# Performance work log

Hardware: AMD Instinct MI355X
Metric: run time of the kernel (lower is better)

## Reference

```python
import jax, jax.numpy as jnp
import numpy as np


def setup_inputs() -> dict:
    key = jax.random.key(0)
    k1, k2 = jax.random.split(key, 2)
    B, N, D = 8, 2048, 1024
    x = jax.random.normal(k1, (B, N, D), dtype=jnp.float32)
    # Linear(D, 3D): weight stored as [in, out] for x @ W
    W_qkv = jax.random.normal(k2, (D, 3 * D), dtype=jnp.float32) * (D ** -0.5)
    b_qkv = jnp.zeros((3 * D,), dtype=jnp.float32)
    return {"x": x, "W_qkv": W_qkv, "b_qkv": b_qkv}


def reference(x, W_qkv, b_qkv):
    D = x.shape[-1]
    scale = D ** -0.5
    qkv = x @ W_qkv + b_qkv                      # [B, N, 3D]
    q, k, v = jnp.split(qkv, 3, axis=-1)         # each [B, N, D]
    # attention scores: note original scales AFTER matmul (same math)
    atten = jnp.einsum('bnd,bmd->bnm', q, k) * scale  # [B, N, N]
    atten = jax.nn.softmax(atten, axis=-1)
    out = jnp.einsum('bnm,bmd->bnd', atten, v)   # [B, N, D]
    return out
```

## Files before the change

kernel.cpp:

```cpp
#include <hip/hip_runtime.h>
#include <hip/hip_bf16.h>


typedef __attribute__((ext_vector_type(8))) short bf16x8;
typedef __attribute__((ext_vector_type(4))) float f32x4;
typedef __attribute__((ext_vector_type(8))) unsigned short u16x8;
typedef __attribute__((address_space(1))) const unsigned int gu32;
typedef __attribute__((address_space(3))) unsigned int lu32;

__device__ __forceinline__ unsigned short f2bf(float f) {
  union { float f; unsigned int u; } v; v.f = f;
  unsigned int r = v.u + 0x7fffu + ((v.u >> 16) & 1u);
  return (unsigned short)(r >> 16);
}
__device__ __forceinline__ void cp16(const unsigned short* g, unsigned short* l) {
  __builtin_amdgcn_global_load_lds((gu32*)g, (lu32*)l, 16, 0, 0);
}

__global__ __launch_bounds__(256) void prep(const float* __restrict__ x,
                                            unsigned short* __restrict__ xb,
                                            const float* __restrict__ W,
                                            unsigned short* __restrict__ Wt,
                                            float* __restrict__ rowsum) {
  __shared__ unsigned short tile[64][72];
  int bid = blockIdx.x, t = threadIdx.x;
  if (bid < 8192) {
    long i = ((long)bid * 256 + t) * 8;
    float4 a = *(const float4*)(x + i);
    float4 b = *(const float4*)(x + i + 4);
    u16x8 o;
    o[0] = f2bf(a.x); o[1] = f2bf(a.y); o[2] = f2bf(a.z); o[3] = f2bf(a.w);
    o[4] = f2bf(b.x); o[5] = f2bf(b.y); o[6] = f2bf(b.z); o[7] = f2bf(b.w);
    *(u16x8*)(xb + i) = o;
  } else if (bid < 8960) {
    int wb = bid - 8192;
    int fb = wb % 48, db = wb / 48;
#pragma unroll
    for (int it = 0; it < 4; it++) {
      int c = t + it * 256;
      int r = c >> 4, c4 = (c & 15) * 4;
      float4 v = *(const float4*)(W + (long)(db * 64 + r) * 3072 + fb * 64 + c4);
      tile[r][c4 + 0] = f2bf(v.x); tile[r][c4 + 1] = f2bf(v.y);
      tile[r][c4 + 2] = f2bf(v.z); tile[r][c4 + 3] = f2bf(v.w);
    }
    __syncthreads();
#pragma unroll
    for (int it = 0; it < 2; it++) {
      int c = t + it * 256;
      int r2 = c >> 3, k8 = (c & 7) * 8;
      u16x8 o;
#pragma unroll
      for (int j = 0; j < 8; j++) o[j] = tile[k8 + j][r2];
      *(u16x8*)(Wt + (long)(fb * 64 + r2) * 1024 + db * 64 + k8) = o;
    }
  } else {
    rowsum[(bid - 8960) * 256 + t] = 0.f;
  }
}

template <int MODE, int SWZ>
__global__ __launch_bounds__(256) void gemm_nt(
    const unsigned short* __restrict__ A, const unsigned short* __restrict__ B,
    float* __restrict__ C, const float* __restrict__ bias, int Ncols, int K, float scale,
    unsigned short* __restrict__ qp, unsigned short* __restrict__ kp,
    unsigned short* __restrict__ vp, float* __restrict__ rsum,
    long strA, long strB, long strC) {
  __shared__ __align__(16) unsigned short As[128 * 64];
  __shared__ __align__(16) unsigned short Bs[128 * 64];
  const int tid = threadIdx.x;
  const int lane = tid & 63, wave = tid >> 6;
  const int quad = lane >> 4, l16 = lane & 15;
  const int bz = blockIdx.z;
  int mt, nt;
  if (SWZ == 0) {
    mt = blockIdx.y; nt = blockIdx.x;
  } else {
    int bid = blockIdx.x;
    int w = bid & 15, st = bid >> 4;
    constexpr int NSUP = SWZ / 4;
    mt = (st / NSUP) * 4 + (w >> 2);
    nt = (st % NSUP) * 4 + (w & 3);
  }
  const long m0 = (long)mt * 128;
  const int n0 = nt * 128;
  const int wm = (wave >> 1) * 64, wn = (wave & 1) * 64;
  const int w8 = wave * 8;
  const int lr = lane >> 3;
  const int swz = (lane & 7) ^ lr;

  f32x4 zero = {0.f, 0.f, 0.f, 0.f};
  f32x4 acc[4][4];
#pragma unroll
  for (int i = 0; i < 4; i++)
#pragma unroll
    for (int j = 0; j < 4; j++) acc[i][j] = zero;

  const unsigned short* aSt = A + (long)bz * strA + (m0 + w8 + lr) * (long)K + swz * 8;
  const unsigned short* bSt = B + (long)bz * strB + ((long)(n0 + w8 + lr)) * K + swz * 8;
  unsigned short* lA = As + (w8 * 64) + lane * 8;
  unsigned short* lB = Bs + (w8 * 64) + lane * 8;

  for (int k0 = 0; k0 < K; k0 += 64) {
    __syncthreads();
#pragma unroll
    for (int j = 0; j < 4; j++) {
      cp16(aSt + (long)j * 32 * K + k0, lA + j * 32 * 64);
      cp16(bSt + (long)j * 32 * K + k0, lB + j * 32 * 64);
    }
    __syncthreads();
#pragma unroll
    for (int h = 0; h < 2; h++) {
      bf16x8 af[4], bfr[4];
#pragma unroll
      for (int i = 0; i < 4; i++) {
        int row = wm + i * 16 + l16;
        af[i] = *(const bf16x8*)(As + row * 64 + (((h << 2) | quad) ^ (row & 7)) * 8);
      }
#pragma unroll
      for (int j = 0; j < 4; j++) {
        int row = wn + j * 16 + l16;
        bfr[j] = *(const bf16x8*)(Bs + row * 64 + (((h << 2) | quad) ^ (row & 7)) * 8);
      }
#pragma unroll
      for (int i = 0; i < 4; i++)
#pragma unroll
        for (int j = 0; j < 4; j++)
          acc[i][j] = __builtin_amdgcn_mfma_f32_16x16x32_bf16(af[i], bfr[j], acc[i][j], 0, 0, 0);
    }
  }

  if (MODE == 1) {
#pragma unroll
    for (int j = 0; j < 4; j++) {
      int fg = n0 + wn + j * 16 + l16;
      float bv = bias[fg];
      if (fg < 2048) {
        unsigned short* outp = (fg < 1024) ? qp : kp;
        int fo = fg & 1023;
#pragma unroll
        for (int i = 0; i < 4; i++)
#pragma unroll
          for (int r = 0; r < 4; r++) {
            long t = m0 + wm + i * 16 + quad * 4 + r;
            outp[t * 1024 + fo] = f2bf(acc[i][j][r] + bv);
          }
      } else {
        int d = fg - 2048;
#pragma unroll
        for (int i = 0; i < 4; i++)
#pragma unroll
          for (int r = 0; r < 4; r++) {
            long t = m0 + wm + i * 16 + quad * 4 + r;
            vp[((long)(t >> 11) * 1024 + d) * 2048 + (t & 2047)] = f2bf(acc[i][j][r] + bv);
          }
      }
    }
  } else if (MODE == 3) {
    unsigned short* Co = qp + (long)bz * strC;
    float* rs = rsum + bz * 2048;
#pragma unroll
    for (int i = 0; i < 4; i++)
#pragma unroll
      for (int r = 0; r < 4; r++) {
        long gm = m0 + wm + i * 16 + quad * 4 + r;
        float psum = 0.f;
#pragma unroll
        for (int j = 0; j < 4; j++) {
          float e = __expf(acc[i][j][r] * scale);
          psum += e;
          Co[gm * Ncols + n0 + wn + j * 16 + l16] = f2bf(e);
        }
        psum += __shfl_xor(psum, 1);
        psum += __shfl_xor(psum, 2);
        psum += __shfl_xor(psum, 4);
        psum += __shfl_xor(psum, 8);
        if (l16 == 0) atomicAdd(rs + gm, psum);
      }
  } else {
    float* Co = C + (long)bz * strC;
    const float* rs = rsum + bz * 2048;
#pragma unroll
    for (int i = 0; i < 4; i++)
#pragma unroll
      for (int r = 0; r < 4; r++) {
        long gm = m0 + wm + i * 16 + quad * 4 + r;
        float inv = 1.0f / rs[gm];
#pragma unroll
        for (int j = 0; j < 4; j++)
          Co[gm * Ncols + n0 + wn + j * 16 + l16] = acc[i][j][r] * inv;
      }
  }
}

extern "C" void kernel_launch(void* const* d_in, const int* in_sizes, int n_in,
                              void* d_out, int out_size, void* d_ws, size_t ws_size,
                              hipStream_t stream) {
  const float* x = (const float*)d_in[0];
  const float* W = (const float*)d_in[1];
  const float* bq = (const float*)d_in[2];
  float* out = (float*)d_out;
  char* ws = (char*)d_ws;
  const long MB = 1L << 20;
  unsigned short* Q  = (unsigned short*)(ws);
  unsigned short* Kb = (unsigned short*)(ws + 32 * MB);
  unsigned short* Vt = (unsigned short*)(ws + 64 * MB);
  unsigned short* xb = (unsigned short*)(ws + 96 * MB);
  unsigned short* Wt = (unsigned short*)(ws + 128 * MB);
  unsigned short* E  = (unsigned short*)(ws + 96 * MB);
  float* rowsum      = (float*)(ws + 160 * MB);

  prep<<<9024, 256, 0, stream>>>(x, xb, W, Wt, rowsum);
  gemm_nt<1, 0><<<dim3(24, 128, 1), 256, 0, stream>>>(xb, Wt, nullptr, bq, 3072, 1024, 1.0f,
                                                      Q, Kb, Vt, nullptr, 0, 0, 0);
  gemm_nt<3, 16><<<dim3(256, 1, 8), 256, 0, stream>>>(Q, Kb, nullptr, nullptr, 2048, 1024,
                                                      0.03125f, E, nullptr, nullptr, rowsum,
                                                      2048L * 1024, 2048L * 1024, 2048L * 2048);
  gemm_nt<4, 8><<<dim3(128, 1, 8), 256, 0, stream>>>(E, Vt, out, nullptr, 1024, 2048, 1.0f,
                                                     nullptr, nullptr, nullptr, rowsum,
                                                     2048L * 2048, 1024L * 2048, 2048L * 1024);
}
```

Measured before the change: 402.6 us.

## Use 256x256 double-buffered GEMM tiles with interleaved async LDS prefetch

Replaces the 128x128 single-buffered GEMM with a 512-thread kernel that computes 256x256 output tiles per block. It keeps two LDS buffers and issues global-to-LDS copies for the next K-tiles between MFMA phases, using explicit waitcnt, barriers and s_setprio. The launch grids and tile swizzles for all three GEMMs are adjusted to match. The goal is more data reuse per LDS load and latency hiding for the global loads. In exchange the kernel uses much more LDS and registers, which lowers occupancy, and the attention GEMMs now launch fewer blocks.

```diff
diff --git a/kernel.cpp b/kernel.cpp
--- a/kernel.cpp
+++ b/kernel.cpp
@@ -59,17 +59,18 @@
 }
 
 template <int MODE, int SWZ>
-__global__ __launch_bounds__(256) void gemm_nt(
+__global__ __launch_bounds__(512, 2) void gemm256(
     const unsigned short* __restrict__ A, const unsigned short* __restrict__ B,
     float* __restrict__ C, const float* __restrict__ bias, int Ncols, int K, float scale,
     unsigned short* __restrict__ qp, unsigned short* __restrict__ kp,
     unsigned short* __restrict__ vp, float* __restrict__ rsum,
     long strA, long strB, long strC) {
-  __shared__ __align__(16) unsigned short As[128 * 64];
-  __shared__ __align__(16) unsigned short Bs[128 * 64];
+  __shared__ __align__(16) unsigned short As[2][256 * 64];
+  __shared__ __align__(16) unsigned short Bs[2][256 * 64];
   const int tid = threadIdx.x;
   const int lane = tid & 63, wave = tid >> 6;
   const int quad = lane >> 4, l16 = lane & 15;
+  const int lr = lane >> 3, lc = lane & 7;
   const int bz = blockIdx.z;
   int mt, nt;
   if (SWZ == 0) {
@@ -77,81 +78,130 @@
   } else {
     int bid = blockIdx.x;
     int w = bid & 15, st = bid >> 4;
-    constexpr int NSUP = SWZ / 4;
+    constexpr int NSUP = (SWZ >= 4) ? (SWZ / 4) : 1;
     mt = (st / NSUP) * 4 + (w >> 2);
     nt = (st % NSUP) * 4 + (w & 3);
   }
-  const long m0 = (long)mt * 128;
-  const int n0 = nt * 128;
-  const int wm = (wave >> 1) * 64, wn = (wave & 1) * 64;
-  const int w8 = wave * 8;
-  const int lr = lane >> 3;
-  const int swz = (lane & 7) ^ lr;
-
+  const long m0 = (long)mt * 256;
+  const int n0 = nt * 256;
+  const int wm128 = (wave >> 2) * 128;
+  const int wn64 = (wave & 3) * 64;
+  const int NT = K >> 6, mask = NT - 1;
+
+  const unsigned short* __restrict__ Ab = A + (long)bz * strA;
+  const unsigned short* __restrict__ Bb = B + (long)bz * strB;
+
+  unsigned int aSrc[4], bSrc[4];
+  int aOff[4], bOff[4];
+  {
+    const int auL[4] = {0, 128, 64, 192}, auH[4] = {32, 160, 96, 224};
+    const int buL[4] = {0, 128, 32, 160}, buH[4] = {64, 192, 96, 224};
+    const bool wlo = wave < 4;
+    const int w8 = (wave & 3) * 8;
+    const int sc = (lc ^ lr) * 8;
+#pragma unroll
+    for (int u = 0; u < 4; u++) {
+      int ra = (wlo ? auL[u] : auH[u]) + w8 + lr;
+      int rb = (wlo ? buL[u] : buH[u]) + w8 + lr;
+      aSrc[u] = (unsigned int)(((int)m0 + ra) * K + sc);
+      bSrc[u] = (unsigned int)((n0 + rb) * K + sc);
+      aOff[u] = ra * 64 + lc * 8;
+      bOff[u] = rb * 64 + lc * 8;
+    }
+  }
+
+#define SA(u, bb, tt) cp16(Ab + aSrc[u] + (tt) * 64, &As[bb][aOff[u]])
+#define SB(u, bb, tt) cp16(Bb + bSrc[u] + (tt) * 64, &Bs[bb][bOff[u]])
+
+  f32x4 acc[8][4];
   f32x4 zero = {0.f, 0.f, 0.f, 0.f};
-  f32x4 acc[4][4];
-#pragma unroll
-  for (int i = 0; i < 4; i++)
+#pragma unroll
+  for (int i = 0; i < 8; i++)
 #pragma unroll
     for (int j = 0; j < 4; j++) acc[i][j] = zero;
-
-  const unsigned short* aSt = A + (long)bz * strA + (m0 + w8 + lr) * (long)K + swz * 8;
-  const unsigned short* bSt = B + (long)bz * strB + ((long)(n0 + w8 + lr)) * K + swz * 8;
-  unsigned short* lA = As + (w8 * 64) + lane * 8;
-  unsigned short* lB = Bs + (w8 * 64) + lane * 8;
-
-  for (int k0 = 0; k0 < K; k0 += 64) {
-    __syncthreads();
+  bf16x8 am[4][2], bn[4][2];
+
+  SA(0, 0, 0); SA(1, 0, 0); SB(0, 0, 0); SB(1, 0, 0);
+  SA(2, 0, 0); SA(3, 0, 0); SB(2, 0, 0); SB(3, 0, 0);
+  SA(0, 1, 1); SA(1, 1, 1); SB(0, 1, 1); SB(1, 1, 1);
+  SA(2, 1, 1); SA(3, 1, 1);
+  asm volatile("s_waitcnt vmcnt(6)" ::: "memory");
+  __builtin_amdgcn_s_barrier();
+
+#define RD_A(bb, mg)                                                                        \
+  _Pragma("unroll") for (int ii = 0; ii < 4; ii++) {                                        \
+    int row = wm128 + ((mg) * 4 + ii) * 16 + l16;                                           \
+    _Pragma("unroll") for (int h = 0; h < 2; h++)                                           \
+      am[ii][h] = *(const bf16x8*)(&As[bb][row * 64 + ((((h << 2) | quad)) ^ (row & 7)) * 8]); \
+  }
+#define RD_B(bb, ng)                                                                        \
+  _Pragma("unroll") for (int jj = 0; jj < 2; jj++) {                                        \
+    int row = wn64 + ((ng) * 2 + jj) * 16 + l16;                                            \
+    _Pragma("unroll") for (int h = 0; h < 2; h++)                                           \
+      bn[(ng) * 2 + jj][h] = *(const bf16x8*)(&Bs[bb][row * 64 + ((((h << 2) | quad)) ^ (row & 7)) * 8]); \
+  }
+#define MM(mg, ng)                                                                          \
+  _Pragma("unroll") for (int ii = 0; ii < 4; ii++)                                          \
+    _Pragma("unroll") for (int jj = 0; jj < 2; jj++)                                        \
+      _Pragma("unroll") for (int h = 0; h < 2; h++)                                         \
+        acc[(mg) * 4 + ii][(ng) * 2 + jj] = __builtin_amdgcn_mfma_f32_16x16x32_bf16(        \
+            am[ii][h], bn[(ng) * 2 + jj][h], acc[(mg) * 4 + ii][(ng) * 2 + jj], 0, 0, 0);
+#define BARRIER __builtin_amdgcn_s_barrier()
+#define LGKM0 asm volatile("s_waitcnt lgkmcnt(0)" ::: "memory")
+#define PRIO1 __builtin_amdgcn_s_setprio(1)
+#define PRIO0 __builtin_amdgcn_s_setprio(0)
+
+#define TILE(bb, tt)                                                                        \
+  {                                                                                         \
+    const int t1_ = ((tt) + 1) & mask, t2_ = ((tt) + 2) & mask;                             \
+                                          \
+    RD_A(bb, 0); RD_B(bb, 0);                                                               \
+    SB(2, (bb) ^ 1, t1_); SB(3, (bb) ^ 1, t1_);                                             \
+    BARRIER; LGKM0; PRIO1; MM(0, 0); PRIO0; BARRIER;                                        \
+                     \
+    RD_B(bb, 1);                                                                            \
+    SA(0, bb, t2_); SA(1, bb, t2_);                                                         \
+    BARRIER; LGKM0; PRIO1; MM(0, 1); PRIO0; BARRIER;                                        \
+                                     \
+    RD_A(bb, 1);                                                                            \
+    SB(0, bb, t2_); SB(1, bb, t2_);                                                         \
+    BARRIER; LGKM0; PRIO1; MM(1, 0); PRIO0; BARRIER;                                        \
+           \
+    SA(2, bb, t2_); SA(3, bb, t2_);                                                         \
+    BARRIER; PRIO1; MM(1, 1); PRIO0;                                                        \
+    asm volatile("s_waitcnt vmcnt(6)" ::: "memory");                                        \
+    BARRIER;                                                                                \
+  }
+
+#pragma unroll 1
+  for (int t = 0; t < NT; t += 2) {
+    TILE(0, t);
+    TILE(1, t + 1);
+  }
+
+  if (MODE == 1) {
 #pragma unroll
     for (int j = 0; j < 4; j++) {
-      cp16(aSt + (long)j * 32 * K + k0, lA + j * 32 * 64);
-      cp16(bSt + (long)j * 32 * K + k0, lB + j * 32 * 64);
-    }
-    __syncthreads();
-#pragma unroll
-    for (int h = 0; h < 2; h++) {
-      bf16x8 af[4], bfr[4];
-#pragma unroll
-      for (int i = 0; i < 4; i++) {
-        int row = wm + i * 16 + l16;
-        af[i] = *(const bf16x8*)(As + row * 64 + (((h << 2) | quad) ^ (row & 7)) * 8);
-      }
-#pragma unroll
-      for (int j = 0; j < 4; j++) {
-        int row = wn + j * 16 + l16;
-        bfr[j] = *(const bf16x8*)(Bs + row * 64 + (((h << 2) | quad) ^ (row & 7)) * 8);
-      }
-#pragma unroll
-      for (int i = 0; i < 4; i++)
-#pragma unroll
-        for (int j = 0; j < 4; j++)
-          acc[i][j] = __builtin_amdgcn_mfma_f32_16x16x32_bf16(af[i], bfr[j], acc[i][j], 0, 0, 0);
-    }
-  }
-
-  if (MODE == 1) {
-#pragma unroll
-    for (int j = 0; j < 4; j++) {
-      int fg = n0 + wn + j * 16 + l16;
+      int fg = n0 + wn64 + j * 16 + l16;
       float bv = bias[fg];
       if (fg < 2048) {
         unsigned short* outp = (fg < 1024) ? qp : kp;
         int fo = fg & 1023;
 #pragma unroll
-        for (int i = 0; i < 4; i++)
+        for (int i = 0; i < 8; i++)
 #pragma unroll
           for (int r = 0; r < 4; r++) {
-            long t = m0 + wm + i * 16 + quad * 4 + r;
-            outp[t * 1024 + fo] = f2bf(acc[i][j][r] + bv);
+            long trow = m0 + wm128 + i * 16 + quad * 4 + r;
+            outp[trow * 1024 + fo] = f2bf(acc[i][j][r] + bv);
           }
       } else {
         int d = fg - 2048;
 #pragma unroll
-        for (int i = 0; i < 4; i++)
+        for (int i = 0; i < 8; i++)
 #pragma unroll
           for (int r = 0; r < 4; r++) {
-            long t = m0 + wm + i * 16 + quad * 4 + r;
-            vp[((long)(t >> 11) * 1024 + d) * 2048 + (t & 2047)] = f2bf(acc[i][j][r] + bv);
+            long trow = m0 + wm128 + i * 16 + quad * 4 + r;
+            vp[((long)(trow >> 11) * 1024 + d) * 2048 + (trow & 2047)] = f2bf(acc[i][j][r] + bv);
           }
       }
     }
@@ -159,16 +209,16 @@
     unsigned short* Co = qp + (long)bz * strC;
     float* rs = rsum + bz * 2048;
 #pragma unroll
-    for (int i = 0; i < 4; i++)
+    for (int i = 0; i < 8; i++)
 #pragma unroll
       for (int r = 0; r < 4; r++) {
-        long gm = m0 + wm + i * 16 + quad * 4 + r;
+        long gm = m0 + wm128 + i * 16 + quad * 4 + r;
         float psum = 0.f;
 #pragma unroll
         for (int j = 0; j < 4; j++) {
           float e = __expf(acc[i][j][r] * scale);
           psum += e;
-          Co[gm * Ncols + n0 + wn + j * 16 + l16] = f2bf(e);
+          Co[gm * Ncols + n0 + wn64 + j * 16 + l16] = f2bf(e);
         }
         psum += __shfl_xor(psum, 1);
         psum += __shfl_xor(psum, 2);
@@ -180,16 +230,27 @@
     float* Co = C + (long)bz * strC;
     const float* rs = rsum + bz * 2048;
 #pragma unroll
-    for (int i = 0; i < 4; i++)
+    for (int i = 0; i < 8; i++)
 #pragma unroll
       for (int r = 0; r < 4; r++) {
-        long gm = m0 + wm + i * 16 + quad * 4 + r;
+        long gm = m0 + wm128 + i * 16 + quad * 4 + r;
         float inv = 1.0f / rs[gm];
 #pragma unroll
         for (int j = 0; j < 4; j++)
-          Co[gm * Ncols + n0 + wn + j * 16 + l16] = acc[i][j][r] * inv;
+          Co[gm * Ncols + n0 + wn64 + j * 16 + l16] = acc[i][j][r] * inv;
       }
   }
+  asm volatile("s_waitcnt vmcnt(0)" ::: "memory");
+#undef SA
+#undef SB
+#undef RD_A
+#undef RD_B
+#undef MM
+#undef TILE
+#undef BARRIER
+#undef LGKM0
+#undef PRIO1
+#undef PRIO0
 }
 
 extern "C" void kernel_launch(void* const* d_in, const int* in_sizes, int n_in,
@@ -210,12 +271,12 @@
   float* rowsum      = (float*)(ws + 160 * MB);
 
   prep<<<9024, 256, 0, stream>>>(x, xb, W, Wt, rowsum);
-  gemm_nt<1, 0><<<dim3(24, 128, 1), 256, 0, stream>>>(xb, Wt, nullptr, bq, 3072, 1024, 1.0f,
+  gemm256<1, 12><<<dim3(768, 1, 1), 512, 0, stream>>>(xb, Wt, nullptr, bq, 3072, 1024, 1.0f,
                                                       Q, Kb, Vt, nullptr, 0, 0, 0);
-  gemm_nt<3, 16><<<dim3(256, 1, 8), 256, 0, stream>>>(Q, Kb, nullptr, nullptr, 2048, 1024,
-                                                      0.03125f, E, nullptr, nullptr, rowsum,
-                                                      2048L * 1024, 2048L * 1024, 2048L * 2048);
-  gemm_nt<4, 8><<<dim3(128, 1, 8), 256, 0, stream>>>(E, Vt, out, nullptr, 1024, 2048, 1.0f,
-                                                     nullptr, nullptr, nullptr, rowsum,
-                                                     2048L * 2048, 1024L * 2048, 2048L * 1024);
-}
+  gemm256<3, 8><<<dim3(64, 1, 8), 512, 0, stream>>>(Q, Kb, nullptr, nullptr, 2048, 1024,
+                                                    0.03125f, E, nullptr, nullptr, rowsum,
+                                                    2048L * 1024, 2048L * 1024, 2048L * 2048);
+  gemm256<4, 4><<<dim3(32, 1, 8), 512, 0, stream>>>(E, Vt, out, nullptr, 1024, 2048, 1.0f,
+                                                    nullptr, nullptr, nullptr, rowsum,
+                                                    2048L * 2048, 1024L * 2048, 2048L * 1024);
+}
```

Measured after the change: 390.3 us. 3.0% less time.
